# Kernel optimization log

Measured on AMD Instinct MI355X. Metric: run time of the kernel, lower is better.

The kernel has to match this reference:

```python
import jax, jax.numpy as jnp
from jax import lax
import numpy as np


def setup_inputs() -> dict:
    key = jax.random.key(0)
    k1, k2, k3 = jax.random.split(key, 3)
    B, X, Y, Z = 8, 128, 128, 128
    P = 64  # total persons across the batch
    feature = jax.random.normal(k1, (B, X, Y, Z), dtype=jnp.float32)
    # float batch indices in [0, B)
    batch_index = jnp.floor(jax.random.uniform(k2, (P,), dtype=jnp.float32) * B)
    # positions inside the voxel grid extent
    person_pos = jax.random.uniform(k3, (P, 3), dtype=jnp.float32) * jnp.array([X - 1, Y - 1, Z - 1], jnp.float32)
    min_loc_xyz = jnp.zeros((3,), jnp.float32)
    loc_delta_xyz = jnp.ones((3,), jnp.float32)
    return {"feature": feature, "batch_index": batch_index, "person_pos": person_pos,
            "min_loc_xyz": min_loc_xyz, "loc_delta_xyz": loc_delta_xyz}


def reference(feature, batch_index, person_pos, min_loc_xyz, loc_delta_xyz):
    B, X, Y, Z = feature.shape
    max_idx = jnp.array([X - 1, Y - 1, Z - 1], jnp.float32)
    # PersonPosToIndexes: world coords -> clipped voxel indices (round via +0.5 cast)
    idx = jnp.clip((person_pos - min_loc_xyz) / loc_delta_xyz, 0.0, max_idx)  # [P,3]
    full = jnp.concatenate([batch_index[:, None], idx], axis=-1)  # [P,4]
    ii = (full + 0.5).astype(jnp.int32)
    # PersonPosToHeatMap: sparse scatter of ones into dense volume
    heat = jnp.zeros(feature.shape, feature.dtype).at[ii[:, 0], ii[:, 1], ii[:, 2], ii[:, 3]].set(1.0)
    # HeatMapToWeights: 3x3x3 max-pool dilation (SAME, stride 1)
    dil = lax.reduce_window(heat, jnp.float32(-jnp.inf), lax.max,
                            (1, 3, 3, 3), (1, 1, 1, 1), 'SAME')
    nr_persons = jnp.sum(heat, axis=(1, 2, 3))  # [B]
    nr_positions = jnp.float32(X * Y * Z)
    scale_neg = (nr_persons * 27.0 / nr_positions)[:, None, None, None]
    scale_pos = (1.0 - nr_persons / nr_positions)[:, None, None, None]
    weights = (1.0 - dil) * scale_neg + heat * scale_pos
    # weighted MSE reduced per batch element, normalized by person count
    se = (feature - heat) ** 2
    loss = jnp.sum(se * weights, axis=(1, 2, 3)) / nr_persons
    return loss
```

## Files before the change

kernel.cpp:

```cpp
#include <hip/hip_runtime.h>

#define BATCH     8
#define DIM       128
#define NVOX      (BATCH * DIM * DIM * DIM)
#define NPERSON   64
#define THREADS   256
#define FLOATS_PER_BLOCK 8192
#define NBLOCK1   (NVOX / FLOATS_PER_BLOCK)
#define TSIZE     4096
#define EMPTYK    0xFFFFFFFFu

#define WS_DIL   2048
#define WS_CORR  2056
#define WS_POS   2064
#define WS_NR    2072

__global__ __launch_bounds__(THREADS) void person_loss_main(
    const float* __restrict__ feature,
    const float* __restrict__ batch_index,
    const float* __restrict__ person_pos,
    const float* __restrict__ min_loc,
    const float* __restrict__ delta,
    float* __restrict__ ws)
{
    __shared__ unsigned keys[NPERSON];
    __shared__ int      uniq[NPERSON];
    __shared__ float    lDil[BATCH], lCorr[BATCH], lPos[BATCH];
    __shared__ int      lNr[BATCH];
    __shared__ unsigned table[TSIZE];
    __shared__ float    red[4];

    const int tid  = threadIdx.x;
    const int bid  = blockIdx.x;
    const int lane = tid & 63, wave = tid >> 6;

    if (bid < NBLOCK1) {
        const float4* f4 = (const float4*)feature;
        const size_t base = (size_t)bid * (FLOATS_PER_BLOCK / 4);
        float acc = 0.f;
#pragma unroll
        for (int j = 0; j < 8; ++j) {
            float4 v = f4[base + (size_t)j * THREADS + tid];
            acc += v.x * v.x + v.y * v.y + v.z * v.z + v.w * v.w;
        }
        for (int off = 32; off > 0; off >>= 1) acc += __shfl_down(acc, off, 64);
        if (lane == 0) red[wave] = acc;
        __syncthreads();
        if (tid == 0) ws[bid] = red[0] + red[1] + red[2] + red[3];
        return;
    }

    if (tid < BATCH) { lDil[tid] = 0.f; lCorr[tid] = 0.f; lPos[tid] = 0.f; lNr[tid] = 0; }
    for (int s = tid; s < TSIZE; s += THREADS) table[s] = EMPTYK;

    if (tid < NPERSON) {
        const int p = tid;
        const int b = (int)(batch_index[p] + 0.5f);
        float vx = (person_pos[p * 3 + 0] - min_loc[0]) / delta[0];
        float vy = (person_pos[p * 3 + 1] - min_loc[1]) / delta[1];
        float vz = (person_pos[p * 3 + 2] - min_loc[2]) / delta[2];
        vx = fminf(fmaxf(vx, 0.f), (float)(DIM - 1));
        vy = fminf(fmaxf(vy, 0.f), (float)(DIM - 1));
        vz = fminf(fmaxf(vz, 0.f), (float)(DIM - 1));
        const int x = (int)(vx + 0.5f);
        const int y = (int)(vy + 0.5f);
        const int z = (int)(vz + 0.5f);
        keys[p] = ((unsigned)b << 21) | ((unsigned)x << 14) | ((unsigned)y << 7) | (unsigned)z;
    }
    __syncthreads();

    if (tid < NPERSON) {
        int u = 1;
        for (int q = 0; q < tid; ++q)
            if (keys[q] == keys[tid]) { u = 0; break; }
        uniq[tid] = u;
        if (u) atomicAdd(&lNr[keys[tid] >> 21], 1);
    }
    __syncthreads();

    for (int w = tid; w < NPERSON * 27; w += THREADS) {
        const int p = w / 27;
        if (!uniq[p]) continue;
        const unsigned k = keys[p];
        const int o = w % 27;
        const int x = (int)((k >> 14) & 127) + (o / 9) - 1;
        const int y = (int)((k >> 7) & 127) + ((o / 3) % 3) - 1;
        const int z = (int)(k & 127) + (o % 3) - 1;
        if ((unsigned)x > (unsigned)(DIM - 1) || (unsigned)y > (unsigned)(DIM - 1) ||
            (unsigned)z > (unsigned)(DIM - 1)) continue;
        const unsigned nk = (k & (7u << 21)) | ((unsigned)x << 14) | ((unsigned)y << 7) | (unsigned)z;
        unsigned h = ((nk * 2654435761u) >> 16) & (TSIZE - 1);
        for (;;) {
            const unsigned old = atomicCAS(&table[h], EMPTYK, nk);
            if (old == EMPTYK || old == nk) break;
            h = (h + 1) & (TSIZE - 1);
        }
    }
    __syncthreads();

    for (int s = tid; s < TSIZE; s += THREADS) {
        const unsigned k = table[s];
        if (k == EMPTYK) continue;
        const int b = k >> 21;
        const int x = (k >> 14) & 127, y = (k >> 7) & 127, z = k & 127;
        const float f = feature[(((size_t)b * DIM + x) * DIM + y) * DIM + z];
        float heat = 0.f;
        for (int q = 0; q < NPERSON; ++q)
            if (keys[q] == k) { heat = 1.f; break; }
        const float d = f - heat;
        atomicAdd(&lDil[b], d * d);
    }

    if (tid < NPERSON && uniq[tid]) {
        const unsigned k = keys[tid];
        const int b = k >> 21;
        const int x = (k >> 14) & 127, y = (k >> 7) & 127, z = k & 127;
        const float f = feature[(((size_t)b * DIM + x) * DIM + y) * DIM + z];
        atomicAdd(&lCorr[b], 1.f - 2.f * f);
        const float d = f - 1.f;
        atomicAdd(&lPos[b], d * d);
    }
    __syncthreads();

    if (tid < BATCH) {
        ws[WS_DIL  + tid] = lDil[tid];
        ws[WS_CORR + tid] = lCorr[tid];
        ws[WS_POS  + tid] = lPos[tid];
        ws[WS_NR   + tid] = (float)lNr[tid];
    }
}

__global__ __launch_bounds__(THREADS) void person_loss_combine(
    const float* __restrict__ ws, float* __restrict__ out)
{
    __shared__ float red[4];
    __shared__ float sS2[BATCH];
    const int tid = threadIdx.x;
    const int lane = tid & 63, wave = tid >> 6;

    for (int b = 0; b < BATCH; ++b) {
        float v = ws[b * (NBLOCK1 / BATCH) + tid];
        for (int off = 32; off > 0; off >>= 1) v += __shfl_down(v, off, 64);
        if (lane == 0) red[wave] = v;
        __syncthreads();
        if (tid == 0) sS2[b] = red[0] + red[1] + red[2] + red[3];
        __syncthreads();
    }

    if (tid < BATCH) {
        const int b = tid;
        const float nr = ws[WS_NR + b];
        const float N = (float)(DIM * DIM * DIM);
        const float scale_neg = nr * 27.f / N;
        const float scale_pos = 1.f - nr / N;
        const float neg = sS2[b] + ws[WS_CORR + b] - ws[WS_DIL + b];
        out[b] = (scale_neg * neg + scale_pos * ws[WS_POS + b]) / nr;
    }
}

extern "C" void kernel_launch(void* const* d_in, const int* in_sizes, int n_in,
                              void* d_out, int out_size, void* d_ws, size_t ws_size,
                              hipStream_t stream)
{
    const float* feature     = (const float*)d_in[0];
    const float* batch_index = (const float*)d_in[1];
    const float* person_pos  = (const float*)d_in[2];
    const float* min_loc     = (const float*)d_in[3];
    const float* delta       = (const float*)d_in[4];
    float* out = (float*)d_out;
    float* ws  = (float*)d_ws;

    person_loss_main<<<NBLOCK1 + 1, THREADS, 0, stream>>>(
        feature, batch_index, person_pos, min_loc, delta, ws);
    person_loss_combine<<<1, THREADS, 0, stream>>>(ws, out);
}
```

Baseline: 117.9 us.

## Run person block first and batch its scattered feature gathers via heat-bit table

Moves the person/hash-table work to block 0 so it is scheduled early instead of as the tail block after all reduction blocks. Marks heat voxels with a flag bit in the hash table instead of scanning all person keys per entry, and issues the table-driven feature loads in batches of eight so their latencies overlap. The dedup loop is unrolled with a fixed trip count. This targets the serial latency tail of the single irregular block, at the cost of extra register use and an added table-marking pass.

```diff
diff --git a/kernel.cpp b/kernel.cpp
--- a/kernel.cpp
+++ b/kernel.cpp
@@ -9,6 +9,8 @@
 #define NBLOCK1   (NVOX / FLOATS_PER_BLOCK)
 #define TSIZE     4096
 #define EMPTYK    0xFFFFFFFFu
+#define KEYMASK   0x00FFFFFFu
+#define HEATBIT   0x40000000u
 
 #define WS_DIL   2048
 #define WS_CORR  2056
@@ -34,9 +36,9 @@
     const int bid  = blockIdx.x;
     const int lane = tid & 63, wave = tid >> 6;
 
-    if (bid < NBLOCK1) {
+    if (bid != 0) {
         const float4* f4 = (const float4*)feature;
-        const size_t base = (size_t)bid * (FLOATS_PER_BLOCK / 4);
+        const size_t base = (size_t)(bid - 1) * (FLOATS_PER_BLOCK / 4);
         float acc = 0.f;
 #pragma unroll
         for (int j = 0; j < 8; ++j) {
@@ -46,7 +48,7 @@
         for (int off = 32; off > 0; off >>= 1) acc += __shfl_down(acc, off, 64);
         if (lane == 0) red[wave] = acc;
         __syncthreads();
-        if (tid == 0) ws[bid] = red[0] + red[1] + red[2] + red[3];
+        if (tid == 0) ws[bid - 1] = red[0] + red[1] + red[2] + red[3];
         return;
     }
 
@@ -70,11 +72,14 @@
     __syncthreads();
 
     if (tid < NPERSON) {
+        const unsigned mykey = keys[tid];
         int u = 1;
-        for (int q = 0; q < tid; ++q)
-            if (keys[q] == keys[tid]) { u = 0; break; }
+#pragma unroll
+        for (int q = 0; q < NPERSON; ++q) {
+            if (q < tid && keys[q] == mykey) u = 0;
+        }
         uniq[tid] = u;
-        if (u) atomicAdd(&lNr[keys[tid] >> 21], 1);
+        if (u) atomicAdd(&lNr[mykey >> 21], 1);
     }
     __syncthreads();
 
@@ -92,33 +97,54 @@
         unsigned h = ((nk * 2654435761u) >> 16) & (TSIZE - 1);
         for (;;) {
             const unsigned old = atomicCAS(&table[h], EMPTYK, nk);
-            if (old == EMPTYK || old == nk) break;
+            if (old == EMPTYK || (old & KEYMASK) == nk) break;
             h = (h + 1) & (TSIZE - 1);
         }
     }
     __syncthreads();
-
-    for (int s = tid; s < TSIZE; s += THREADS) {
-        const unsigned k = table[s];
-        if (k == EMPTYK) continue;
-        const int b = k >> 21;
-        const int x = (k >> 14) & 127, y = (k >> 7) & 127, z = k & 127;
-        const float f = feature[(((size_t)b * DIM + x) * DIM + y) * DIM + z];
-        float heat = 0.f;
-        for (int q = 0; q < NPERSON; ++q)
-            if (keys[q] == k) { heat = 1.f; break; }
-        const float d = f - heat;
-        atomicAdd(&lDil[b], d * d);
-    }
 
     if (tid < NPERSON && uniq[tid]) {
         const unsigned k = keys[tid];
-        const int b = k >> 21;
-        const int x = (k >> 14) & 127, y = (k >> 7) & 127, z = k & 127;
-        const float f = feature[(((size_t)b * DIM + x) * DIM + y) * DIM + z];
-        atomicAdd(&lCorr[b], 1.f - 2.f * f);
-        const float d = f - 1.f;
-        atomicAdd(&lPos[b], d * d);
+        unsigned h = ((k * 2654435761u) >> 16) & (TSIZE - 1);
+        for (;;) {
+            const unsigned e = table[h];
+            if (e != EMPTYK && (e & KEYMASK) == k) { atomicOr(&table[h], HEATBIT); break; }
+            h = (h + 1) & (TSIZE - 1);
+        }
+    }
+    __syncthreads();
+
+#pragma unroll
+    for (int c = 0; c < 2; ++c) {
+        unsigned e[8];
+#pragma unroll
+        for (int j = 0; j < 8; ++j)
+            e[j] = table[(c * 8 + j) * THREADS + tid];
+
+        float f[8];
+#pragma unroll
+        for (int j = 0; j < 8; ++j) {
+            f[j] = 0.f;
+            if (e[j] != EMPTYK) {
+                const unsigned k = e[j];
+                const int b = (k >> 21) & 7;
+                const int x = (k >> 14) & 127, y = (k >> 7) & 127, z = k & 127;
+                f[j] = feature[(((size_t)b * DIM + x) * DIM + y) * DIM + z];
+            }
+        }
+#pragma unroll
+        for (int j = 0; j < 8; ++j) {
+            if (e[j] == EMPTYK) continue;
+            const int b = (e[j] >> 21) & 7;
+            const float heat = (e[j] & HEATBIT) ? 1.f : 0.f;
+            const float d = f[j] - heat;
+            atomicAdd(&lDil[b], d * d);
+            if (e[j] & HEATBIT) {
+                atomicAdd(&lCorr[b], 1.f - 2.f * f[j]);
+                const float dp = f[j] - 1.f;
+                atomicAdd(&lPos[b], dp * dp);
+            }
+        }
     }
     __syncthreads();
 
```

After: 102.5 us. -13.1%, faster.
